# Kernel tuning notes

Measured on AMD Instinct MI355X. Metric: run time of the kernel, lower is better.

## Reference

```python
import jax, jax.numpy as jnp
import numpy as np

N = 100000
E = 3200000
IN_C = 512
HID = 64
LOC = 64
GLOB = 64
OUT_C = 40
K = 10
ALPHA = 0.1


def setup_inputs() -> dict:
    key = jax.random.key(0)
    ks = jax.random.split(key, 10)
    batch_x = jax.random.normal(ks[0], (N, IN_C), dtype=jnp.float32)
    edge_index = jax.random.randint(ks[1], (2, E), 0, N, dtype=jnp.int32)
    glob_emb = jax.random.normal(ks[2], (N, GLOB), dtype=jnp.float32)
    # Linear params (Glorot-ish scale)
    W1 = jax.random.normal(ks[3], (IN_C, HID), dtype=jnp.float32) / np.sqrt(IN_C)
    b1 = jnp.zeros((HID,), dtype=jnp.float32)
    W2 = jax.random.normal(ks[4], (HID, LOC), dtype=jnp.float32) / np.sqrt(HID)
    b2 = jnp.zeros((LOC,), dtype=jnp.float32)
    # GPR-GNN PPR init coefficients: temp[k] = alpha*(1-alpha)^k, temp[K] = (1-alpha)^K
    temp_np = ALPHA * (1.0 - ALPHA) ** np.arange(K + 1)
    temp_np[-1] = (1.0 - ALPHA) ** K
    temp = jnp.asarray(temp_np, dtype=jnp.float32)
    Wl = jax.random.normal(ks[5], (LOC + GLOB, OUT_C), dtype=jnp.float32) / np.sqrt(LOC + GLOB)
    bl = jnp.zeros((OUT_C,), dtype=jnp.float32)
    return {"batch_x": batch_x, "edge_index": edge_index, "glob_emb": glob_emb,
            "W1": W1, "b1": b1, "W2": W2, "b2": b2, "temp": temp, "Wl": Wl, "bl": bl}


def _gcn_norm(edge_index, num_nodes):
    # add self loops (weight 1), symmetric normalization like PyG gcn_norm
    loops = jnp.arange(num_nodes, dtype=edge_index.dtype)
    row = jnp.concatenate([edge_index[0], loops])  # sources
    col = jnp.concatenate([edge_index[1], loops])  # targets
    w = jnp.ones(row.shape[0], dtype=jnp.float32)
    deg = jax.ops.segment_sum(w, col, num_segments=num_nodes)
    dinv = jnp.where(deg > 0, jax.lax.rsqrt(jnp.maximum(deg, 1.0)), 0.0)
    norm = dinv[row] * dinv[col]
    return row, col, norm


def reference(batch_x, edge_index, glob_emb, W1, b1, W2, b2, temp, Wl, bl):
    # eval mode: all dropouts are identity
    x = jax.nn.relu(batch_x @ W1 + b1)
    x = x @ W2 + b2  # [N, LOC]
    n = x.shape[0]
    row, col, norm = _gcn_norm(edge_index, n)
    hidden = x * temp[0]
    for k in range(K):
        # message: norm * x[src]; aggregate: scatter-add at target
        x = jax.ops.segment_sum(norm[:, None] * x[row], col, num_segments=n)
        hidden = hidden + temp[k + 1] * x
    emb = jnp.concatenate([hidden, glob_emb], axis=1)  # [N, LOC+GLOB]
    return emb @ Wl + bl
```

## Files before the change

kernel.cpp:

```cpp
#include <hip/hip_runtime.h>


typedef _Float16 half8 __attribute__((ext_vector_type(8)));
typedef _Float16 f16x8 __attribute__((ext_vector_type(8)));
typedef _Float16 f16x4 __attribute__((ext_vector_type(4)));
typedef float f32x4 __attribute__((ext_vector_type(4)));


__global__ __launch_bounds__(256) void bucketA_kernel(const int* __restrict__ edge,
                                                      unsigned long long* __restrict__ barr,
                                                      int* __restrict__ bcnt,
                                                      int E, int cap) {
  __shared__ int lcnt[64];
  __shared__ int lbase[64];
  int t = threadIdx.x;
  if (t < 64) lcnt[t] = 0;
  __syncthreads();
  int e0 = blockIdx.x * 2048 + t;
  int rk[8];
  int bk[8];
  unsigned long long pk[8];
#pragma unroll
  for (int i = 0; i < 8; ++i) {
    int e = e0 + i * 256;
    int s = 0, c = 0;
    if (e < E) { s = edge[e]; c = edge[E + e]; }
    int b = c >> 11;
    bk[i] = b;
    pk[i] = ((unsigned long long)(unsigned)c << 32) | (unsigned)s;
    if (e < E) rk[i] = atomicAdd(&lcnt[b], 1);
    else rk[i] = -1;
  }
  __syncthreads();
  if (t < 64 && lcnt[t] > 0) lbase[t] = atomicAdd(&bcnt[t], lcnt[t]);
  __syncthreads();
#pragma unroll
  for (int i = 0; i < 8; ++i)
    if (rk[i] >= 0)
      barr[(size_t)bk[i] * cap + lbase[bk[i]] + rk[i]] = pk[i];
}

__global__ __launch_bounds__(256) void countB_kernel(const unsigned long long* __restrict__ barr,
                                                     const int* __restrict__ bcnt,
                                                     int* __restrict__ counts,
                                                     float* __restrict__ dinv,
                                                     int cap, int Nn) {
  __shared__ int h[2048];
  int b = blockIdx.x;
  int t = threadIdx.x;
  for (int i = t; i < 2048; i += 256) h[i] = 0;
  __syncthreads();
  int cnt = bcnt[b];
  const unsigned long long* ep = barr + (size_t)b * cap;
  int base = b << 11;
  for (int e = t; e < cnt; e += 256) {
    int c = (int)(ep[e] >> 32);
    atomicAdd(&h[c - base], 1);
  }
  __syncthreads();
  for (int i = t; i < 2048; i += 256) {
    int node = base + i;
    if (node < Nn) {
      int d = h[i];
      counts[node] = d;
      dinv[node] = rsqrtf((float)(d + 1));
    }
  }
}

__global__ __launch_bounds__(256) void fillB_kernel(const unsigned long long* __restrict__ barr,
                                                    const int* __restrict__ bcnt,
                                                    const int* __restrict__ rowptr,
                                                    int* __restrict__ cursor,
                                                    int* __restrict__ srcoff,
                                                    int cap, int nb, int nbx, int cpb) {
  int i = blockIdx.x;
  int x = i & 7;
  int j = i >> 3;
  int bslot = j % nbx;
  int chunk = j / nbx;
  int b = x + 8 * bslot;
  if (b >= nb) return;
  int cnt = bcnt[b];
  int lo = (int)((long long)cnt * chunk / cpb);
  int hi = (int)((long long)cnt * (chunk + 1) / cpb);
  const unsigned long long* ep = barr + (size_t)b * cap;
  for (int e = lo + threadIdx.x; e < hi; e += 256) {
    unsigned long long pk = ep[e];
    int s = (int)(unsigned)pk;
    int c = (int)(pk >> 32);
    int p = rowptr[c] + atomicAdd(&cursor[c], 1);
    srcoff[p] = s;
  }
}

__global__ __launch_bounds__(256) void scanA_kernel(const int* __restrict__ counts,
                                                    int* __restrict__ incl,
                                                    int* __restrict__ partials, int Nn) {
  __shared__ int sbuf[256];
  int t = threadIdx.x;
  int base = blockIdx.x * 1024 + t * 4;
  int a0 = (base + 0 < Nn) ? counts[base + 0] : 0;
  int a1 = (base + 1 < Nn) ? counts[base + 1] : 0;
  int a2 = (base + 2 < Nn) ? counts[base + 2] : 0;
  int a3 = (base + 3 < Nn) ? counts[base + 3] : 0;
  int tot = a0 + a1 + a2 + a3;
  sbuf[t] = tot;
  __syncthreads();
  for (int off = 1; off < 256; off <<= 1) {
    int v = (t >= off) ? sbuf[t - off] : 0;
    __syncthreads();
    sbuf[t] += v;
    __syncthreads();
  }
  int excl = sbuf[t] - tot;
  if (base + 0 < Nn) incl[base + 0] = excl + a0;
  if (base + 1 < Nn) incl[base + 1] = excl + a0 + a1;
  if (base + 2 < Nn) incl[base + 2] = excl + a0 + a1 + a2;
  if (base + 3 < Nn) incl[base + 3] = excl + tot;
  if (t == 255) partials[blockIdx.x] = sbuf[255];
}

__global__ void scanB_kernel(const int* __restrict__ partials,
                             int* __restrict__ chunkoff, int B) {
  __shared__ int sbuf[256];
  int t = threadIdx.x;
  int v = (t < B) ? partials[t] : 0;
  sbuf[t] = v;
  __syncthreads();
  for (int off = 1; off < 256; off <<= 1) {
    int u = (t >= off) ? sbuf[t - off] : 0;
    __syncthreads();
    sbuf[t] += u;
    __syncthreads();
  }
  chunkoff[t] = sbuf[t] - v;
}

__global__ __launch_bounds__(256) void finalize_scan_kernel(const int* __restrict__ incl,
                                                            const int* __restrict__ chunkoff,
                                                            int* __restrict__ rowptr, int Nn) {
  int i = blockIdx.x * 256 + threadIdx.x;
  if (i < Nn) rowptr[i + 1] = incl[i] + chunkoff[i >> 10];
  if (i == 0) rowptr[0] = 0;
}


__global__ __launch_bounds__(256) void w1t_kernel(const float* __restrict__ W1,
                                                  _Float16* __restrict__ W1T) {
  int idx = blockIdx.x * 256 + threadIdx.x;
  int col = idx >> 9;
  int k = idx & 511;
  W1T[col * 512 + k] = (_Float16)W1[k * 64 + col];
}


__global__ __launch_bounds__(256) void mlp1_mfma_kernel(const float* __restrict__ X,
                                                        const _Float16* __restrict__ W1T,
                                                        const float* __restrict__ b1,
                                                        float* __restrict__ H, int Nn) {
  __shared__ _Float16 sX[64][88];
  __shared__ _Float16 sWT[64][88];
  int t = threadIdx.x;
  int m0 = blockIdx.x * 64;
  int lane = t & 63, w = t >> 6;
  f32x4 acc[4];
#pragma unroll
  for (int i = 0; i < 4; ++i) acc[i] = (f32x4){0.f, 0.f, 0.f, 0.f};
  int l15 = lane & 15;
  int kgrp = (lane >> 4) * 8;

  for (int k0 = 0; k0 < 512; k0 += 64) {
#pragma unroll
    for (int i = 0; i < 4; ++i) {
      int lin = t + i * 256;
      int m = lin >> 4;
      int kq = (lin & 15) * 4;
      float4 v = make_float4(0.f, 0.f, 0.f, 0.f);
      if (m0 + m < Nn) v = *(const float4*)&X[(size_t)(m0 + m) * 512 + k0 + kq];
      f16x4 h4 = {(_Float16)v.x, (_Float16)v.y, (_Float16)v.z, (_Float16)v.w};
      *(f16x4*)&sX[m][kq] = h4;
    }
#pragma unroll
    for (int i = 0; i < 2; ++i) {
      int c = t + i * 256;
      int col = c >> 3;
      int k8 = (c & 7) * 8;
      f16x8 v = *(const f16x8*)&W1T[col * 512 + k0 + k8];
      *(f16x8*)&sWT[col][k8] = v;
    }
    __syncthreads();
#pragma unroll
    for (int kc = 0; kc < 2; ++kc) {
      f16x8 a = *(const f16x8*)&sX[16 * w + l15][kc * 32 + kgrp];
#pragma unroll
      for (int c = 0; c < 4; ++c) {
        f16x8 b = *(const f16x8*)&sWT[c * 16 + l15][kc * 32 + kgrp];
        acc[c] = __builtin_amdgcn_mfma_f32_16x16x32_f16(a, b, acc[c], 0, 0, 0);
      }
    }
    __syncthreads();
  }
  int rbase = m0 + 16 * w + (lane >> 4) * 4;
#pragma unroll
  for (int c = 0; c < 4; ++c) {
    float bias = b1[c * 16 + l15];
#pragma unroll
    for (int r = 0; r < 4; ++r) {
      int row = rbase + r;
      if (row < Nn) H[(size_t)row * 64 + c * 16 + l15] = fmaxf(acc[c][r] + bias, 0.f);
    }
  }
}


__global__ void computeM_kernel(const float* __restrict__ W2, const float* __restrict__ Wl,
                                const float* __restrict__ b2, float* __restrict__ Mm,
                                float* __restrict__ cv) {
  int t = threadIdx.x;
  for (int idx = t; idx < 2560; idx += 256) {
    int k = idx / 40, o = idx - k * 40;
    float s = 0.f;
    for (int j = 0; j < 64; ++j) s += W2[k * 64 + j] * Wl[j * 40 + o];
    Mm[idx] = s;
  }
  if (t < 40) {
    float s = 0.f;
    for (int j = 0; j < 64; ++j) s += b2[j] * Wl[j * 40 + t];
    cv[t] = s;
  }
}

__global__ void zeropad_kernel(char* __restrict__ yA, char* __restrict__ yB,
                               int Nn, int yboff) {
  int t = threadIdx.x;
  if (t < 32) {
    ((_Float16*)(yA + (size_t)Nn * 64))[t] = (_Float16)0.f;
    ((_Float16*)(yB + (size_t)Nn * 64))[t] = (_Float16)0.f;
  } else if (t < 40) {
    ((_Float16*)(yA + yboff + (size_t)Nn * 16))[t - 32] = (_Float16)0.f;
    ((_Float16*)(yB + yboff + (size_t)Nn * 16))[t - 32] = (_Float16)0.f;
  }
}


__global__ __launch_bounds__(256) void z0_kernel(const float* __restrict__ H,
                                                 const float* __restrict__ Mm,
                                                 const float* __restrict__ cv,
                                                 const float* __restrict__ dinv,
                                                 const float* __restrict__ temp,
                                                 char* __restrict__ y0,
                                                 float* __restrict__ hid, int Nn, int yboff) {
  __shared__ float sM[2624];
  __shared__ float sc[40];
  int t = threadIdx.x;
  for (int i = t; i < 2560; i += 256) sM[i] = Mm[i];
  for (int i = 2560 + t; i < 2624; i += 256) sM[i] = 0.f;
  if (t < 40) sc[t] = cv[t];
  __syncthreads();
  int wid = t >> 6, lane = t & 63;
  int node = blockIdx.x * 4 + wid;
  if (node < Nn) {
    float h = H[(size_t)node * 64 + lane];
    float acc = (lane < 40) ? sc[lane] : 0.f;
#pragma unroll 8
    for (int k = 0; k < 64; ++k) acc += __shfl(h, k) * sM[k * 40 + lane];
    if (lane < 40) {
      float di = dinv[node];
      float y = di * acc;
      if (lane < 32)
        ((_Float16*)(y0 + (size_t)node * 64))[lane] = (_Float16)y;
      else
        ((_Float16*)(y0 + yboff + (size_t)node * 16))[lane - 32] = (_Float16)y;
      hid[(size_t)node * 40 + lane] = temp[0] * y;
    }
  }
}


__global__ __launch_bounds__(256) void prop_kernel(const char* __restrict__ yin,
                                                   char* __restrict__ yout,
                                                   float* __restrict__ hid,
                                                   const int* __restrict__ srcoff,
                                                   const int* __restrict__ rowptr,
                                                   const float* __restrict__ dinv,
                                                   const float* __restrict__ temp,
                                                   int kidx, int Nn, int yboff) {
  __shared__ float red[4][60][8];
  int t = threadIdx.x, wid = t >> 6, lane = t & 63;
  int node = blockIdx.x * 4 + wid;
  int sub = lane / 5;
  int cl = lane - sub * 5;
  int lmul = (cl == 4) ? 16 : 64;
  int ladd = (cl == 4) ? yboff : (cl << 4);
  float a0 = 0.f, a1 = 0.f, a2 = 0.f, a3 = 0.f, a4 = 0.f, a5 = 0.f, a6 = 0.f, a7 = 0.f;
  if (node < Nn) {
    int start = rowptr[node], end = rowptr[node + 1];
    for (int b0 = start; b0 < end; b0 += 60) {
      int j = b0 + lane;
      int msrc = (lane < 60 && j < end) ? srcoff[j] : Nn;
#pragma unroll
      for (int tt = 0; tt < 5; ++tt) {
        int n = __shfl(msrc, tt * 12 + sub);
        half8 v = *(const half8*)(yin + (size_t)(n * lmul + ladd));
        a0 += (float)v[0]; a1 += (float)v[1]; a2 += (float)v[2]; a3 += (float)v[3];
        a4 += (float)v[4]; a5 += (float)v[5]; a6 += (float)v[6]; a7 += (float)v[7];
      }
    }
  }
  if (lane < 60) {
    red[wid][lane][0] = a0; red[wid][lane][1] = a1;
    red[wid][lane][2] = a2; red[wid][lane][3] = a3;
    red[wid][lane][4] = a4; red[wid][lane][5] = a5;
    red[wid][lane][6] = a6; red[wid][lane][7] = a7;
  }
  __syncthreads();
  if (node < Nn && lane < 5) {
    float s[8];
#pragma unroll
    for (int i = 0; i < 8; ++i) s[i] = 0.f;
#pragma unroll
    for (int g = 0; g < 12; ++g)
#pragma unroll
      for (int i = 0; i < 8; ++i) s[i] += red[wid][g * 5 + lane][i];
    float di = dinv[node];
    float m = di * di;
    int lm2 = (lane == 4) ? 16 : 64;
    int la2 = (lane == 4) ? yboff : (lane << 4);
    half8 self = *(const half8*)(yin + (size_t)(node * lm2 + la2));
    float yn[8];
    half8 outv;
#pragma unroll
    for (int i = 0; i < 8; ++i) {
      yn[i] = m * (s[i] + (float)self[i]);
      outv[i] = (_Float16)yn[i];
    }
    *(half8*)(yout + (size_t)(node * lm2 + la2)) = outv;
    float tk = temp[kidx];
    float* hp = &hid[(size_t)node * 40 + lane * 8];
    float4 h0 = *(float4*)hp;
    float4 h1 = *(float4*)(hp + 4);
    h0.x += tk * yn[0]; h0.y += tk * yn[1]; h0.z += tk * yn[2]; h0.w += tk * yn[3];
    h1.x += tk * yn[4]; h1.y += tk * yn[5]; h1.z += tk * yn[6]; h1.w += tk * yn[7];
    *(float4*)hp = h0;
    *(float4*)(hp + 4) = h1;
  }
}


__global__ __launch_bounds__(256) void final_kernel(const float* __restrict__ glob,
                                                    const float* __restrict__ Wl,
                                                    const float* __restrict__ bl,
                                                    const float* __restrict__ hid,
                                                    const int* __restrict__ counts,
                                                    const float* __restrict__ dinv,
                                                    float* __restrict__ out, int Nn) {
  __shared__ float sW[2624];
  __shared__ float sb[40];
  int t = threadIdx.x;
  for (int i = t; i < 2560; i += 256) sW[i] = Wl[2560 + i];
  for (int i = 2560 + t; i < 2624; i += 256) sW[i] = 0.f;
  if (t < 40) sb[t] = bl[t];
  __syncthreads();
  int wid = t >> 6, lane = t & 63;
  int node = blockIdx.x * 4 + wid;
  if (node < Nn) {
    float g = glob[(size_t)node * 64 + lane];
    float acc = (lane < 40) ? sb[lane] : 0.f;
#pragma unroll 8
    for (int k = 0; k < 64; ++k) acc += __shfl(g, k) * sW[k * 40 + lane];
    if (lane < 40) {
      float sc = (float)(counts[node] + 1) * dinv[node];
      out[(size_t)node * 40 + lane] = sc * hid[(size_t)node * 40 + lane] + acc;
    }
  }
}


extern "C" void kernel_launch(void* const* d_in, const int* in_sizes, int n_in,
                              void* d_out, int out_size, void* d_ws, size_t ws_size,
                              hipStream_t stream) {
  const float* X    = (const float*)d_in[0];
  const int*   edge = (const int*)d_in[1];
  const float* glob = (const float*)d_in[2];
  const float* W1   = (const float*)d_in[3];
  const float* b1   = (const float*)d_in[4];
  const float* W2   = (const float*)d_in[5];
  const float* b2   = (const float*)d_in[6];
  const float* temp = (const float*)d_in[7];
  const float* Wl   = (const float*)d_in[8];
  const float* bl   = (const float*)d_in[9];
  float* out = (float*)d_out;

  int Nn = in_sizes[0] / 512;
  int E  = in_sizes[1] / 2;
  int Kk = in_sizes[7] - 1;

  char* p = (char*)d_ws;
  auto alloc = [&](size_t bytes) {
    char* r = p;
    p += (bytes + 255) & ~(size_t)255;
    return r;
  };
  int*   counts   = (int*)alloc((size_t)Nn * 4);
  int*   rowptr   = (int*)alloc((size_t)(Nn + 1) * 4);
  int*   incl     = (int*)alloc((size_t)Nn * 4);
  int*   partials = (int*)alloc(256 * 4);
  int*   chunkoff = (int*)alloc(256 * 4);
  int*   cursor   = (int*)alloc((size_t)Nn * 4);
  float* dinv     = (float*)alloc((size_t)Nn * 4);
  int*   srcoff   = (int*)alloc((size_t)E * 4);
  float* Hbuf     = (float*)alloc((size_t)Nn * 64 * 4);
  float* Mm       = (float*)alloc(2560 * 4);
  float* cv       = (float*)alloc(64 * 4);
  _Float16* W1T   = (_Float16*)alloc(64 * 512 * 2);
  int yboff = (Nn + 1) * 64;
  size_t ybytes = (size_t)(Nn + 1) * 80;
  char*  yA       = (char*)alloc(ybytes);
  char*  yB       = (char*)alloc(ybytes);
  float* hid      = (float*)alloc((size_t)Nn * 40 * 4);

  int nb  = (Nn + 2047) >> 11;
  int nbx = (nb + 7) / 8;
  int cap = E / nb + E / (nb * 8) + 1024;
  unsigned long long* barr = (unsigned long long*)alloc((size_t)nb * cap * 8);
  int* bcnt = (int*)alloc(64 * 4);

  hipMemsetAsync(cursor, 0, (size_t)Nn * 4, stream);
  hipMemsetAsync(bcnt, 0, 64 * 4, stream);

  bucketA_kernel<<<(E + 2047) / 2048, 256, 0, stream>>>(edge, barr, bcnt, E, cap);
  countB_kernel<<<nb, 256, 0, stream>>>(barr, bcnt, counts, dinv, cap, Nn);
  int B = (Nn + 1023) / 1024;
  scanA_kernel<<<B, 256, 0, stream>>>(counts, incl, partials, Nn);
  scanB_kernel<<<1, 256, 0, stream>>>(partials, chunkoff, B);
  finalize_scan_kernel<<<(Nn + 255) / 256, 256, 0, stream>>>(incl, chunkoff, rowptr, Nn);
  int cpb = 32;
  fillB_kernel<<<8 * nbx * cpb, 256, 0, stream>>>(barr, bcnt, rowptr, cursor, srcoff,
                                                  cap, nb, nbx, cpb);

  w1t_kernel<<<128, 256, 0, stream>>>(W1, W1T);
  mlp1_mfma_kernel<<<(Nn + 63) / 64, 256, 0, stream>>>(X, W1T, b1, Hbuf, Nn);
  computeM_kernel<<<1, 256, 0, stream>>>(W2, Wl, b2, Mm, cv);
  zeropad_kernel<<<1, 64, 0, stream>>>(yA, yB, Nn, yboff);

  int nodeBlocks = (Nn + 3) / 4;
  z0_kernel<<<nodeBlocks, 256, 0, stream>>>(Hbuf, Mm, cv, dinv, temp, yA, hid, Nn, yboff);

  char* yin = yA;
  char* yout = yB;
  for (int k = 1; k <= Kk; ++k) {
    prop_kernel<<<nodeBlocks, 256, 0, stream>>>(yin, yout, hid, srcoff, rowptr, dinv,
                                                temp, k, Nn, yboff);
    char* tmpp = yin; yin = yout; yout = tmpp;
  }

  final_kernel<<<nodeBlocks, 256, 0, stream>>>(glob, Wl, bl, hid, counts, dinv, out, Nn);
}
```

Before: 1.392 ms.

## Fuse K propagation steps into one persistent cooperative kernel with grid sync

Replaces the per-iteration prop_kernel launches with a single cooperative persistent kernel that loops over the K propagation steps, using a grid-wide sync between steps and ping-ponging buffers internally. The block-level __syncthreads is replaced by an LDS waitcnt since each wave only reads its own reduction slot. This removes kernel launch gaps, but it caps occupancy to the co-resident grid and adds grid barrier cost, which may reduce latency hiding for the gather-heavy loop.

After: 2.963 ms. 113% more time.

```diff
diff --git a/kernel.cpp b/kernel.cpp
--- a/kernel.cpp
+++ b/kernel.cpp
@@ -1,4 +1,7 @@
 #include <hip/hip_runtime.h>
+#include <hip/hip_cooperative_groups.h>
+
+namespace cg = cooperative_groups;
 
 
 typedef _Float16 half8 __attribute__((ext_vector_type(8)));
@@ -278,72 +281,80 @@
 }
 
 
-__global__ __launch_bounds__(256) void prop_kernel(const char* __restrict__ yin,
-                                                   char* __restrict__ yout,
-                                                   float* __restrict__ hid,
-                                                   const int* __restrict__ srcoff,
-                                                   const int* __restrict__ rowptr,
-                                                   const float* __restrict__ dinv,
-                                                   const float* __restrict__ temp,
-                                                   int kidx, int Nn, int yboff) {
+__global__ __launch_bounds__(256, 4) void prop_fused_kernel(
+    char* __restrict__ yAp, char* __restrict__ yBp,
+    float* __restrict__ hid,
+    const int* __restrict__ srcoff, const int* __restrict__ rowptr,
+    const float* __restrict__ dinv, const float* __restrict__ temp,
+    int Kk, int Nn, int yboff, int ngroups) {
+  cg::grid_group gg = cg::this_grid();
   __shared__ float red[4][60][8];
   int t = threadIdx.x, wid = t >> 6, lane = t & 63;
-  int node = blockIdx.x * 4 + wid;
   int sub = lane / 5;
   int cl = lane - sub * 5;
   int lmul = (cl == 4) ? 16 : 64;
   int ladd = (cl == 4) ? yboff : (cl << 4);
-  float a0 = 0.f, a1 = 0.f, a2 = 0.f, a3 = 0.f, a4 = 0.f, a5 = 0.f, a6 = 0.f, a7 = 0.f;
-  if (node < Nn) {
-    int start = rowptr[node], end = rowptr[node + 1];
-    for (int b0 = start; b0 < end; b0 += 60) {
-      int j = b0 + lane;
-      int msrc = (lane < 60 && j < end) ? srcoff[j] : Nn;
-#pragma unroll
-      for (int tt = 0; tt < 5; ++tt) {
-        int n = __shfl(msrc, tt * 12 + sub);
-        half8 v = *(const half8*)(yin + (size_t)(n * lmul + ladd));
-        a0 += (float)v[0]; a1 += (float)v[1]; a2 += (float)v[2]; a3 += (float)v[3];
-        a4 += (float)v[4]; a5 += (float)v[5]; a6 += (float)v[6]; a7 += (float)v[7];
+  int lm2 = (lane == 4) ? 16 : 64;
+  int la2 = (lane == 4) ? yboff : (lane << 4);
+  const char* yin = yAp;
+  char* yout = yBp;
+  for (int k = 1; k <= Kk; ++k) {
+    float tk = temp[k];
+    for (int grp = blockIdx.x; grp < ngroups; grp += gridDim.x) {
+      int node = grp * 4 + wid;
+      float a0 = 0.f, a1 = 0.f, a2 = 0.f, a3 = 0.f, a4 = 0.f, a5 = 0.f, a6 = 0.f, a7 = 0.f;
+      if (node < Nn) {
+        int start = rowptr[node], end = rowptr[node + 1];
+        for (int b0 = start; b0 < end; b0 += 60) {
+          int j = b0 + lane;
+          int msrc = (lane < 60 && j < end) ? srcoff[j] : Nn;
+#pragma unroll
+          for (int tt = 0; tt < 5; ++tt) {
+            int n = __shfl(msrc, tt * 12 + sub);
+            half8 v = *(const half8*)(yin + (size_t)(n * lmul + ladd));
+            a0 += (float)v[0]; a1 += (float)v[1]; a2 += (float)v[2]; a3 += (float)v[3];
+            a4 += (float)v[4]; a5 += (float)v[5]; a6 += (float)v[6]; a7 += (float)v[7];
+          }
+        }
       }
-    }
-  }
-  if (lane < 60) {
-    red[wid][lane][0] = a0; red[wid][lane][1] = a1;
-    red[wid][lane][2] = a2; red[wid][lane][3] = a3;
-    red[wid][lane][4] = a4; red[wid][lane][5] = a5;
-    red[wid][lane][6] = a6; red[wid][lane][7] = a7;
-  }
-  __syncthreads();
-  if (node < Nn && lane < 5) {
-    float s[8];
-#pragma unroll
-    for (int i = 0; i < 8; ++i) s[i] = 0.f;
-#pragma unroll
-    for (int g = 0; g < 12; ++g)
-#pragma unroll
-      for (int i = 0; i < 8; ++i) s[i] += red[wid][g * 5 + lane][i];
-    float di = dinv[node];
-    float m = di * di;
-    int lm2 = (lane == 4) ? 16 : 64;
-    int la2 = (lane == 4) ? yboff : (lane << 4);
-    half8 self = *(const half8*)(yin + (size_t)(node * lm2 + la2));
-    float yn[8];
-    half8 outv;
-#pragma unroll
-    for (int i = 0; i < 8; ++i) {
-      yn[i] = m * (s[i] + (float)self[i]);
-      outv[i] = (_Float16)yn[i];
-    }
-    *(half8*)(yout + (size_t)(node * lm2 + la2)) = outv;
-    float tk = temp[kidx];
-    float* hp = &hid[(size_t)node * 40 + lane * 8];
-    float4 h0 = *(float4*)hp;
-    float4 h1 = *(float4*)(hp + 4);
-    h0.x += tk * yn[0]; h0.y += tk * yn[1]; h0.z += tk * yn[2]; h0.w += tk * yn[3];
-    h1.x += tk * yn[4]; h1.y += tk * yn[5]; h1.z += tk * yn[6]; h1.w += tk * yn[7];
-    *(float4*)hp = h0;
-    *(float4*)(hp + 4) = h1;
+      if (lane < 60) {
+        red[wid][lane][0] = a0; red[wid][lane][1] = a1;
+        red[wid][lane][2] = a2; red[wid][lane][3] = a3;
+        red[wid][lane][4] = a4; red[wid][lane][5] = a5;
+        red[wid][lane][6] = a6; red[wid][lane][7] = a7;
+      }
+      asm volatile("s_waitcnt lgkmcnt(0)" ::: "memory");
+      __builtin_amdgcn_sched_barrier(0);
+      if (node < Nn && lane < 5) {
+        float s[8];
+#pragma unroll
+        for (int i = 0; i < 8; ++i) s[i] = 0.f;
+#pragma unroll
+        for (int g = 0; g < 12; ++g)
+#pragma unroll
+          for (int i = 0; i < 8; ++i) s[i] += red[wid][g * 5 + lane][i];
+        float di = dinv[node];
+        float m = di * di;
+        half8 self = *(const half8*)(yin + (size_t)(node * lm2 + la2));
+        float yn[8];
+        half8 outv;
+#pragma unroll
+        for (int i = 0; i < 8; ++i) {
+          yn[i] = m * (s[i] + (float)self[i]);
+          outv[i] = (_Float16)yn[i];
+        }
+        *(half8*)(yout + (size_t)(node * lm2 + la2)) = outv;
+        float* hp = &hid[(size_t)node * 40 + lane * 8];
+        float4 h0 = *(float4*)hp;
+        float4 h1 = *(float4*)(hp + 4);
+        h0.x += tk * yn[0]; h0.y += tk * yn[1]; h0.z += tk * yn[2]; h0.w += tk * yn[3];
+        h1.x += tk * yn[4]; h1.y += tk * yn[5]; h1.z += tk * yn[6]; h1.w += tk * yn[7];
+        *(float4*)hp = h0;
+        *(float4*)(hp + 4) = h1;
+      }
+    }
+    gg.sync();
+    const char* tmpp = yin; yin = yout; yout = (char*)tmpp;
   }
 }
 
@@ -447,13 +458,28 @@
   int nodeBlocks = (Nn + 3) / 4;
   z0_kernel<<<nodeBlocks, 256, 0, stream>>>(Hbuf, Mm, cv, dinv, temp, yA, hid, Nn, yboff);
 
-  char* yin = yA;
-  char* yout = yB;
-  for (int k = 1; k <= Kk; ++k) {
-    prop_kernel<<<nodeBlocks, 256, 0, stream>>>(yin, yout, hid, srcoff, rowptr, dinv,
-                                                temp, k, Nn, yboff);
-    char* tmpp = yin; yin = yout; yout = tmpp;
-  }
+  static int s_grid = 0;
+  if (s_grid == 0) {
+    int bpc = 0;
+    if (hipOccupancyMaxActiveBlocksPerMultiprocessor(
+            &bpc, (const void*)prop_fused_kernel, 256, 0) != hipSuccess || bpc < 1)
+      bpc = 4;
+    int cus = 256;
+    hipDeviceProp_t props;
+    int dev = 0;
+    if (hipGetDevice(&dev) == hipSuccess &&
+        hipGetDeviceProperties(&props, dev) == hipSuccess &&
+        props.multiProcessorCount > 0)
+      cus = props.multiProcessorCount;
+    s_grid = bpc * cus;
+  }
+  int ngroups = nodeBlocks;
+  int grid = s_grid < ngroups ? s_grid : ngroups;
+  void* kargs[] = {(void*)&yA, (void*)&yB, (void*)&hid, (void*)&srcoff,
+                   (void*)&rowptr, (void*)&dinv, (void*)&temp,
+                   (void*)&Kk, (void*)&Nn, (void*)&yboff, (void*)&ngroups};
+  hipLaunchCooperativeKernel((const void*)prop_fused_kernel, dim3(grid), dim3(256),
+                             kargs, 0, stream);
 
   final_kernel<<<nodeBlocks, 256, 0, stream>>>(glob, Wl, bl, hid, counts, dinv, out, Nn);
 }
```
